# Kernel optimization log

Measured on AMD Instinct MI355X. Metric: run time of the kernel, lower is better.

## Reference

```python
import jax, jax.numpy as jnp
import numpy as np

B, NQ, NN, EMB, H, D = 64, 256, 512, 128, 8, 16
SQRT_EMB = float(np.sqrt(EMB))
LOGIT_CLIP = 10.0


def setup_inputs() -> dict:
    key = jax.random.key(0)
    ks = jax.random.split(key, 9)
    encoded_last_node = jax.random.normal(ks[0], (B, NQ, EMB), jnp.float32)
    attr = jax.random.uniform(ks[1], (B, NQ, 1), jnp.float32)  # e.g. remaining load in [0,1]
    encoded_nodes = jax.random.normal(ks[2], (B, NN, EMB), jnp.float32)
    ninf_mask = jnp.where(jax.random.uniform(ks[3], (B, NQ, NN)) < 0.15,
                          -jnp.inf, 0.0).astype(jnp.float32)
    def lin(k, fan_in, fan_out):
        lim = 1.0 / np.sqrt(fan_in)
        return jax.random.uniform(k, (fan_in, fan_out), jnp.float32, -lim, lim)
    Wq_last = lin(ks[4], EMB + 1, H * D)
    Wk = lin(ks[5], EMB, H * D)
    Wv = lin(ks[6], EMB, H * D)
    Wcomb = lin(ks[7], H * D, EMB)
    bcomb = jax.random.uniform(ks[8], (EMB,), jnp.float32, -1.0 / np.sqrt(H * D), 1.0 / np.sqrt(H * D))
    return dict(encoded_last_node=encoded_last_node, attr=attr,
                encoded_nodes=encoded_nodes, ninf_mask=ninf_mask,
                Wq_last=Wq_last, Wk=Wk, Wv=Wv, Wcomb=Wcomb, bcomb=bcomb)


def _heads(x):  # [B, T, H*D] -> [B, H, T, D]
    return x.reshape(x.shape[0], x.shape[1], H, D).transpose(0, 2, 1, 3)


def reference(encoded_last_node, attr, encoded_nodes, ninf_mask,
              Wq_last, Wk, Wv, Wcomb, bcomb):
    # fix fully-masked rows: un-mask index 0 (matches torch mask_inf patch)
    all_inf = jnp.isinf(ninf_mask).all(axis=2)  # [B, NQ]
    ninf_mask = ninf_mask.at[:, :, 0].set(jnp.where(all_inf, 0.0, ninf_mask[:, :, 0]))

    # set_kv
    k = _heads(encoded_nodes @ Wk)  # [B,H,NN,D]
    v = _heads(encoded_nodes @ Wv)  # [B,H,NN,D]

    # q from last node + attr
    q = _heads(jnp.concatenate([encoded_last_node, attr], axis=2) @ Wq_last)  # [B,H,NQ,D]

    # masked multi-head attention
    score = jnp.einsum('bhnd,bhmd->bhnm', q, k) / jnp.sqrt(jnp.float32(D))
    score = score + ninf_mask[:, None, :, :]          # rank3 mask broadcast over heads
    weights = jax.nn.softmax(score, axis=-1)          # [B,H,NQ,NN]
    out = jnp.einsum('bhnm,bhmd->bhnd', weights, v)
    out_concat = out.transpose(0, 2, 1, 3).reshape(B, NQ, H * D)
    mh_atten_out = out_concat @ Wcomb + bcomb         # [B,NQ,EMB]

    # single-head compatibility score + tanh clip + mask + softmax
    score2 = jnp.einsum('bne,bme->bnm', mh_atten_out, encoded_nodes) / SQRT_EMB
    logits = LOGIT_CLIP * jnp.tanh(score2) + ninf_mask
    probs = jax.nn.softmax(logits, axis=2)            # [B,NQ,NN]
    return probs
```

## Files before the change

### kernel.cpp

```cpp
#include <hip/hip_runtime.h>
#include <math.h>

#define NB    64
#define NQn   256
#define NNn   512
#define HDn   128
#define LOG2E 1.44269504088896340736f
#define INV_SQRT_EMB 0.08838834764831845f

__device__ __forceinline__ float4 ldg4(const float* p) {
    return *reinterpret_cast<const float4*>(p);
}

__global__ __launch_bounds__(256, 4)
void mask_transpose(const float* __restrict__ mask, unsigned char* __restrict__ maskT8)
{
    __shared__ float Ms[64 * 65];
    const int tid = threadIdx.x;
    const int b   = blockIdx.x;
    const int q0  = blockIdx.y * 64;
    const int n0  = blockIdx.z * 64;
    const int qg  = tid >> 6;
    const int ln  = tid & 63;

    #pragma unroll
    for (int j = 0; j < 16; ++j) {
        int q = qg * 16 + j;
        Ms[q * 65 + ln] = mask[((size_t)(b * NQn + q0 + q)) * NNn + n0 + ln];
    }
    __syncthreads();

    const int n  = tid >> 2;
    const int qc = (tid & 3) * 16;
    unsigned int u[4] = {0u, 0u, 0u, 0u};
    #pragma unroll
    for (int j = 0; j < 16; ++j) {
        float v = Ms[(qc + j) * 65 + n];
        unsigned int bit = (v != 0.0f) ? 1u : 0u;
        u[j >> 2] |= bit << (8 * (j & 3));
    }
    *reinterpret_cast<uint4*>(maskT8 + ((size_t)(b * NNn + n0 + n)) * NQn + q0 + qc) =
        make_uint4(u[0], u[1], u[2], u[3]);
}

__global__ __launch_bounds__(256, 2)
void proj_kernel(const float* __restrict__ X,
                 const float* __restrict__ W0, const float* __restrict__ W1,
                 const float* __restrict__ wrow, const float* __restrict__ attr,
                 const float* __restrict__ bias,
                 float* __restrict__ Y0, float* __restrict__ Y1)
{
    __shared__ float Xs[64 * 128];
    __shared__ float Wt[64 * 128];
    const int tid = threadIdx.x;
    const int rg = tid >> 4;
    const int cg = tid & 15;
    const int rowblk = blockIdx.x * 64;
    const int colbase = blockIdx.y * 64;

    #pragma unroll
    for (int i = 0; i < 8; ++i) {
        int idx = tid + 256 * i;
        int r = idx >> 5;
        int c4 = idx & 31;
        float4 v = ldg4(X + (rowblk + r) * 128 + c4 * 4);
        *reinterpret_cast<float4*>(&Xs[r * 128 + ((c4 ^ (r & 7)) << 2)]) = v;
    }

    for (int pass = 0; pass < 2; ++pass) {
        if (pass && (W1 == nullptr)) break;
        const float* W = pass ? W1 : W0;
        float* Y = pass ? Y1 : Y0;
        __syncthreads();
        #pragma unroll
        for (int i = 0; i < 32; ++i) {
            int idx = tid + 256 * i;
            int k = idx >> 6;
            int c = idx & 63;
            float w = W[k * 128 + colbase + c];
            Wt[c * 128 + ((((k >> 2) ^ (c & 7)) << 2) | (k & 3))] = w;
        }
        __syncthreads();

        float acc[4][4];
        #pragma unroll
        for (int r = 0; r < 4; ++r)
            #pragma unroll
            for (int c = 0; c < 4; ++c) acc[r][c] = 0.f;

        const int rsw = rg & 7;
        const int csw = cg & 7;
        #pragma unroll 8
        for (int k4 = 0; k4 < 32; ++k4) {
            float4 a[4], bv[4];
            #pragma unroll
            for (int r = 0; r < 4; ++r)
                a[r] = *reinterpret_cast<const float4*>(&Xs[(rg + 16 * r) * 128 + ((k4 ^ rsw) << 2)]);
            #pragma unroll
            for (int c = 0; c < 4; ++c)
                bv[c] = *reinterpret_cast<const float4*>(&Wt[(cg + 16 * c) * 128 + ((k4 ^ csw) << 2)]);
            #pragma unroll
            for (int r = 0; r < 4; ++r)
                #pragma unroll
                for (int c = 0; c < 4; ++c)
                    acc[r][c] += a[r].x * bv[c].x + a[r].y * bv[c].y
                               + a[r].z * bv[c].z + a[r].w * bv[c].w;
        }

        if (attr != nullptr) {
            #pragma unroll
            for (int r = 0; r < 4; ++r) {
                float av = attr[rowblk + rg + 16 * r];
                #pragma unroll
                for (int c = 0; c < 4; ++c)
                    acc[r][c] += av * wrow[colbase + cg + 16 * c];
            }
        }
        #pragma unroll
        for (int r = 0; r < 4; ++r) {
            int row = rowblk + rg + 16 * r;
            #pragma unroll
            for (int c = 0; c < 4; ++c) {
                int col = colbase + cg + 16 * c;
                float o = acc[r][c];
                if (bias != nullptr) o += bias[col];
                Y[row * 128 + col] = o;
            }
        }
    }
}

__global__ __launch_bounds__(256, 2)
void attn_kernel(const float* __restrict__ Q, const float* __restrict__ K,
                 const float* __restrict__ V, const unsigned int* __restrict__ maskTu,
                 float* __restrict__ P0, float* __restrict__ P1,
                 float* __restrict__ P2, float* __restrict__ P3,
                 float* __restrict__ L0, float* __restrict__ L1,
                 float* __restrict__ L2, float* __restrict__ L3)
{
    __shared__ float Ks[32 * 128];
    __shared__ float Vs[32 * 128];
    const int tid  = threadIdx.x;
    const int lane = tid & 63;
    const int h    = blockIdx.z * 4 + (tid >> 6);
    const int b    = blockIdx.x;
    const int ns   = blockIdx.y;
    const int nbase = ns * 128;

    float qv[4][16];
    {
        const float sc = 0.25f * LOG2E;
        #pragma unroll
        for (int qq = 0; qq < 4; ++qq) {
            const float* qp = Q + ((size_t)(b * NQn + 4 * lane + qq)) * 128 + h * 16;
            #pragma unroll
            for (int j = 0; j < 4; ++j) {
                float4 tv = ldg4(qp + 4 * j);
                qv[qq][4 * j + 0] = tv.x * sc;
                qv[qq][4 * j + 1] = tv.y * sc;
                qv[qq][4 * j + 2] = tv.z * sc;
                qv[qq][4 * j + 3] = tv.w * sc;
            }
        }
    }

    float out[4][16];
    #pragma unroll
    for (int qq = 0; qq < 4; ++qq)
        #pragma unroll
        for (int d = 0; d < 16; ++d) out[qq][d] = 0.f;
    float ls[4] = {0.f, 0.f, 0.f, 0.f};

    const unsigned int* mbase = maskTu + (((size_t)(b * NNn + nbase) * NQn) >> 2) + lane;

    const float* kg = K + ((size_t)(b * NNn + nbase)) * 128;
    const float* vg = V + ((size_t)(b * NNn + nbase)) * 128;

    float4 krp[4], vrp[4];
    #pragma unroll
    for (int i = 0; i < 4; ++i) {
        krp[i] = ldg4(kg + (tid + 256 * i) * 4);
        vrp[i] = ldg4(vg + (tid + 256 * i) * 4);
    }

    for (int t = 0; t < 4; ++t) {
        __syncthreads();
        #pragma unroll
        for (int i = 0; i < 4; ++i) {
            *reinterpret_cast<float4*>(&Ks[(tid + 256 * i) * 4]) = krp[i];
            *reinterpret_cast<float4*>(&Vs[(tid + 256 * i) * 4]) = vrp[i];
        }
        __syncthreads();
        if (t < 3) {
            const float* kg2 = kg + (t + 1) * 32 * 128;
            const float* vg2 = vg + (t + 1) * 32 * 128;
            #pragma unroll
            for (int i = 0; i < 4; ++i) {
                krp[i] = ldg4(kg2 + (tid + 256 * i) * 4);
                vrp[i] = ldg4(vg2 + (tid + 256 * i) * 4);
            }
        }

        const float* kbase = &Ks[h * 16];
        const float* vbase = &Vs[h * 16];
        for (int n = 0; n < 32; ++n) {
            const float* kr = kbase + n * 128;
            const float* vr = vbase + n * 128;
            float kf[16], vf[16];
            *reinterpret_cast<float4*>(&kf[0])  = *reinterpret_cast<const float4*>(kr);
            *reinterpret_cast<float4*>(&kf[4])  = *reinterpret_cast<const float4*>(kr + 4);
            *reinterpret_cast<float4*>(&kf[8])  = *reinterpret_cast<const float4*>(kr + 8);
            *reinterpret_cast<float4*>(&kf[12]) = *reinterpret_cast<const float4*>(kr + 12);
            *reinterpret_cast<float4*>(&vf[0])  = *reinterpret_cast<const float4*>(vr);
            *reinterpret_cast<float4*>(&vf[4])  = *reinterpret_cast<const float4*>(vr + 4);
            *reinterpret_cast<float4*>(&vf[8])  = *reinterpret_cast<const float4*>(vr + 8);
            *reinterpret_cast<float4*>(&vf[12]) = *reinterpret_cast<const float4*>(vr + 12);
            unsigned int m4 = mbase[(t * 32 + n) * (NQn / 4)];

            float p[4];
            #pragma unroll
            for (int qq = 0; qq < 4; ++qq) {
                float aP = qv[qq][0]*kf[0] + qv[qq][1]*kf[1] + qv[qq][2]*kf[2] + qv[qq][3]*kf[3];
                float aQ = qv[qq][4]*kf[4] + qv[qq][5]*kf[5] + qv[qq][6]*kf[6] + qv[qq][7]*kf[7];
                float aR = qv[qq][8]*kf[8] + qv[qq][9]*kf[9] + qv[qq][10]*kf[10] + qv[qq][11]*kf[11];
                float aS = qv[qq][12]*kf[12] + qv[qq][13]*kf[13] + qv[qq][14]*kf[14] + qv[qq][15]*kf[15];
                p[qq] = __builtin_amdgcn_exp2f((aP + aQ) + (aR + aS));
            }
            p[0] = (m4 & 0x000000ffu) ? 0.f : p[0];
            p[1] = (m4 & 0x0000ff00u) ? 0.f : p[1];
            p[2] = (m4 & 0x00ff0000u) ? 0.f : p[2];
            p[3] = (m4 & 0xff000000u) ? 0.f : p[3];
            ls[0] += p[0]; ls[1] += p[1]; ls[2] += p[2]; ls[3] += p[3];
            #pragma unroll
            for (int d = 0; d < 16; ++d) {
                out[0][d] += p[0] * vf[d];
                out[1][d] += p[1] * vf[d];
                out[2][d] += p[2] * vf[d];
                out[3][d] += p[3] * vf[d];
            }
        }
    }

    float* P = (ns == 0) ? P0 : (ns == 1) ? P1 : (ns == 2) ? P2 : P3;
    float* L = (ns == 0) ? L0 : (ns == 1) ? L1 : (ns == 2) ? L2 : L3;
    #pragma unroll
    for (int qq = 0; qq < 4; ++qq) {
        float* op = P + ((size_t)(b * NQn + 4 * lane + qq)) * 128 + h * 16;
        *reinterpret_cast<float4*>(op)      = make_float4(out[qq][0],  out[qq][1],  out[qq][2],  out[qq][3]);
        *reinterpret_cast<float4*>(op + 4)  = make_float4(out[qq][4],  out[qq][5],  out[qq][6],  out[qq][7]);
        *reinterpret_cast<float4*>(op + 8)  = make_float4(out[qq][8],  out[qq][9],  out[qq][10], out[qq][11]);
        *reinterpret_cast<float4*>(op + 12) = make_float4(out[qq][12], out[qq][13], out[qq][14], out[qq][15]);
        L[(b * NQn + 4 * lane + qq) * 8 + h] = ls[qq];
    }
}

__global__ __launch_bounds__(256, 2)
void proj_comb_kernel(const float* __restrict__ P0, const float* __restrict__ P1,
                      const float* __restrict__ P2, const float* __restrict__ P3,
                      const float* __restrict__ L0, const float* __restrict__ L1,
                      const float* __restrict__ L2, const float* __restrict__ L3,
                      const float* __restrict__ V,
                      const float* __restrict__ W0, const float* __restrict__ bias,
                      float* __restrict__ Y0)
{
    __shared__ float Xs[64 * 128];
    __shared__ float Wt[64 * 128];
    const int tid = threadIdx.x;
    const int rg = tid >> 4;
    const int cg = tid & 15;
    const int rowblk = blockIdx.x * 64;
    const int colbase = blockIdx.y * 64;

    #pragma unroll
    for (int i = 0; i < 8; ++i) {
        int idx = tid + 256 * i;
        int r = idx >> 5;
        int c4 = idx & 31;
        int row = rowblk + r;
        int hh = c4 >> 2;
        float l = (L0[row * 8 + hh] + L1[row * 8 + hh])
                + (L2[row * 8 + hh] + L3[row * 8 + hh]);
        float4 v;
        if (l == 0.0f) {
            v = ldg4(V + ((size_t)(row >> 8)) * NNn * 128 + c4 * 4);
        } else {
            float4 a = ldg4(P0 + (size_t)row * 128 + c4 * 4);
            float4 c = ldg4(P1 + (size_t)row * 128 + c4 * 4);
            float4 d = ldg4(P2 + (size_t)row * 128 + c4 * 4);
            float4 e = ldg4(P3 + (size_t)row * 128 + c4 * 4);
            float inv = __builtin_amdgcn_rcpf(l);
            v = make_float4((a.x + c.x + d.x + e.x) * inv,
                            (a.y + c.y + d.y + e.y) * inv,
                            (a.z + c.z + d.z + e.z) * inv,
                            (a.w + c.w + d.w + e.w) * inv);
        }
        *reinterpret_cast<float4*>(&Xs[r * 128 + ((c4 ^ (r & 7)) << 2)]) = v;
    }

    __syncthreads();
    #pragma unroll
    for (int i = 0; i < 32; ++i) {
        int idx = tid + 256 * i;
        int k = idx >> 6;
        int c = idx & 63;
        float w = W0[k * 128 + colbase + c];
        Wt[c * 128 + ((((k >> 2) ^ (c & 7)) << 2) | (k & 3))] = w;
    }
    __syncthreads();

    float acc[4][4];
    #pragma unroll
    for (int r = 0; r < 4; ++r)
        #pragma unroll
        for (int c = 0; c < 4; ++c) acc[r][c] = 0.f;

    const int rsw = rg & 7;
    const int csw = cg & 7;
    #pragma unroll 8
    for (int k4 = 0; k4 < 32; ++k4) {
        float4 a[4], bv[4];
        #pragma unroll
        for (int r = 0; r < 4; ++r)
            a[r] = *reinterpret_cast<const float4*>(&Xs[(rg + 16 * r) * 128 + ((k4 ^ rsw) << 2)]);
        #pragma unroll
        for (int c = 0; c < 4; ++c)
            bv[c] = *reinterpret_cast<const float4*>(&Wt[(cg + 16 * c) * 128 + ((k4 ^ csw) << 2)]);
        #pragma unroll
        for (int r = 0; r < 4; ++r)
            #pragma unroll
            for (int c = 0; c < 4; ++c)
                acc[r][c] += a[r].x * bv[c].x + a[r].y * bv[c].y
                           + a[r].z * bv[c].z + a[r].w * bv[c].w;
    }

    #pragma unroll
    for (int r = 0; r < 4; ++r) {
        int row = rowblk + rg + 16 * r;
        #pragma unroll
        for (int c = 0; c < 4; ++c) {
            int col = colbase + cg + 16 * c;
            Y0[row * 128 + col] = acc[r][c] + bias[col];
        }
    }
}

__global__ __launch_bounds__(512, 4)
void final_kernel(const float* __restrict__ MH, const float* __restrict__ EN,
                  const float* __restrict__ mask, float* __restrict__ OUT)
{
    __shared__ float ENs[128 * 128];
    const int tid = threadIdx.x;
    const int qg = tid >> 4;
    const int mg = tid & 15;
    const int b  = blockIdx.x >> 3;
    const int q0 = (blockIdx.x & 7) * 32;

    const float* mhrow = MH + (b * NQn + q0 + qg) * 128;
    float pr[32];
    float psum = 0.f;
    const int msw = mg & 7;

    #pragma unroll
    for (int t = 0; t < 4; ++t) {
        const int m0 = t * 128;
        __syncthreads();
        #pragma unroll
        for (int i = 0; i < 8; ++i) {
            int idx = tid + 512 * i;
            int r = idx >> 5;
            int c4 = idx & 31;
            float4 v = ldg4(EN + (b * NNn + m0 + r) * 128 + c4 * 4);
            *reinterpret_cast<float4*>(&ENs[r * 128 + ((c4 ^ (r & 7)) << 2)]) = v;
        }
        __syncthreads();

        float acc[8];
        #pragma unroll
        for (int c = 0; c < 8; ++c) acc[c] = 0.f;

        #pragma unroll 4
        for (int k4 = 0; k4 < 32; ++k4) {
            float4 a0 = ldg4(mhrow + k4 * 4);
            float4 bv[8];
            #pragma unroll
            for (int c = 0; c < 8; ++c)
                bv[c] = *reinterpret_cast<const float4*>(&ENs[(mg + 16 * c) * 128 + ((k4 ^ msw) << 2)]);
            #pragma unroll
            for (int c = 0; c < 8; ++c)
                acc[c] += a0.x*bv[c].x + a0.y*bv[c].y + a0.z*bv[c].z + a0.w*bv[c].w;
        }

        const float* mrow = mask + (b * NQn + q0 + qg) * NNn + m0;
        #pragma unroll
        for (int c = 0; c < 8; ++c) {
            int m = mg + 16 * c;
            float s2 = acc[c] * INV_SQRT_EMB;
            float e  = __builtin_amdgcn_exp2f(s2 * (2.0f * LOG2E));
            float rc = __builtin_amdgcn_rcpf(e + 1.0f);
            float mv = mrow[m];
            float pv = __builtin_amdgcn_exp2f((mv - 20.0f * rc) * LOG2E);
            pr[t * 8 + c] = pv;
            psum += pv;
        }
    }

    {
        float s = psum;
        s += __shfl_xor(s, 1);
        s += __shfl_xor(s, 2);
        s += __shfl_xor(s, 4);
        s += __shfl_xor(s, 8);
        psum = s;
    }

    float* orow = OUT + (b * NQn + q0 + qg) * NNn;
    if (psum == 0.0f) {
        #pragma unroll
        for (int t = 0; t < 4; ++t)
            #pragma unroll
            for (int c = 0; c < 8; ++c) {
                int m = t * 128 + mg + 16 * c;
                orow[m] = (m == 0) ? 1.0f : 0.0f;
            }
    } else {
        float inv = __builtin_amdgcn_rcpf(psum);
        #pragma unroll
        for (int t = 0; t < 4; ++t)
            #pragma unroll
            for (int c = 0; c < 8; ++c)
                orow[t * 128 + mg + 16 * c] = pr[t * 8 + c] * inv;
    }
}

extern "C" void kernel_launch(void* const* d_in, const int* in_sizes, int n_in,
                              void* d_out, int out_size, void* d_ws, size_t ws_size,
                              hipStream_t stream) {
    const float* enc_last  = (const float*)d_in[0];
    const float* attr      = (const float*)d_in[1];
    const float* enc_nodes = (const float*)d_in[2];
    const float* mask      = (const float*)d_in[3];
    const float* Wq        = (const float*)d_in[4];
    const float* Wk        = (const float*)d_in[5];
    const float* Wv        = (const float*)d_in[6];
    const float* Wcomb     = (const float*)d_in[7];
    const float* bcomb     = (const float*)d_in[8];
    float* out = (float*)d_out;

    float* Kbuf = (float*)d_ws;
    float* Vbuf = Kbuf + (size_t)NB * NNn * 128;
    float* Qbuf = Vbuf + (size_t)NB * NNn * 128;
    float* P0   = Qbuf + (size_t)NB * NQn * 128;
    float* P1   = P0   + (size_t)NB * NQn * 128;
    float* P2   = P1   + (size_t)NB * NQn * 128;
    float* P3   = P2   + (size_t)NB * NQn * 128;
    float* L0   = P3   + (size_t)NB * NQn * 128;
    float* L1   = L0   + (size_t)NB * NQn * 8;
    float* L2   = L1   + (size_t)NB * NQn * 8;
    float* L3   = L2   + (size_t)NB * NQn * 8;
    unsigned char* maskT8 = (unsigned char*)(L3 + (size_t)NB * NQn * 8);
    float* MH   = Qbuf;

    mask_transpose<<<dim3(NB, NQn / 64, NNn / 64), 256, 0, stream>>>(mask, maskT8);
    proj_kernel<<<dim3(NB * NNn / 64, 2), 256, 0, stream>>>(
        enc_nodes, Wk, Wv, nullptr, nullptr, nullptr, Kbuf, Vbuf);
    proj_kernel<<<dim3(NB * NQn / 64, 2), 256, 0, stream>>>(
        enc_last, Wq, nullptr, Wq + 128 * 128, attr, nullptr, Qbuf, nullptr);
    attn_kernel<<<dim3(NB, 4, 2), 256, 0, stream>>>(
        Qbuf, Kbuf, Vbuf, (const unsigned int*)maskT8,
        P0, P1, P2, P3, L0, L1, L2, L3);
    proj_comb_kernel<<<dim3(NB * NQn / 64, 2), 256, 0, stream>>>(
        P0, P1, P2, P3, L0, L1, L2, L3, Vbuf, Wcomb, bcomb, MH);
    final_kernel<<<dim3(NB * NQn / 32), 512, 0, stream>>>(
        MH, enc_nodes, mask, out);
}
```

Before: 248.7 us.

## Split attention over 8 node chunks with all heads per block, enlarge final blocks

The attention kernel now runs all 8 heads in one 512-thread block. Each block loads a shared K/V tile once for every head instead of twice across two head-halves, and the work is split over up to 8 node chunks when the workspace allows it. The register prefetch double-buffering is removed in favour of a direct load-sync-compute loop. The combine kernel sums a variable number of partials, and the final kernel uses 1024-thread blocks covering 64 queries so each staged encoded-node tile is reused by more rows. The risks are lower occupancy from the larger blocks with heavy register use, more partial traffic to reduce, and exposed load latency now that prefetch is gone.

```diff
diff --git a/kernel.cpp b/kernel.cpp
--- a/kernel.cpp
+++ b/kernel.cpp
@@ -130,22 +130,19 @@
     }
 }
 
-__global__ __launch_bounds__(256, 2)
+__global__ __launch_bounds__(512, 2)
 void attn_kernel(const float* __restrict__ Q, const float* __restrict__ K,
                  const float* __restrict__ V, const unsigned int* __restrict__ maskTu,
-                 float* __restrict__ P0, float* __restrict__ P1,
-                 float* __restrict__ P2, float* __restrict__ P3,
-                 float* __restrict__ L0, float* __restrict__ L1,
-                 float* __restrict__ L2, float* __restrict__ L3)
+                 float* __restrict__ Pbase, float* __restrict__ Lbase, int ntiles)
 {
     __shared__ float Ks[32 * 128];
     __shared__ float Vs[32 * 128];
     const int tid  = threadIdx.x;
     const int lane = tid & 63;
-    const int h    = blockIdx.z * 4 + (tid >> 6);
+    const int h    = tid >> 6;
     const int b    = blockIdx.x;
     const int ns   = blockIdx.y;
-    const int nbase = ns * 128;
+    const int nbase = ns * (ntiles * 32);
 
     float qv[4][16];
     {
@@ -173,33 +170,21 @@
 
     const unsigned int* mbase = maskTu + (((size_t)(b * NNn + nbase) * NQn) >> 2) + lane;
 
-    const float* kg = K + ((size_t)(b * NNn + nbase)) * 128;
-    const float* vg = V + ((size_t)(b * NNn + nbase)) * 128;
-
-    float4 krp[4], vrp[4];
-    #pragma unroll
-    for (int i = 0; i < 4; ++i) {
-        krp[i] = ldg4(kg + (tid + 256 * i) * 4);
-        vrp[i] = ldg4(vg + (tid + 256 * i) * 4);
-    }
-
-    for (int t = 0; t < 4; ++t) {
-        __syncthreads();
-        #pragma unroll
-        for (int i = 0; i < 4; ++i) {
-            *reinterpret_cast<float4*>(&Ks[(tid + 256 * i) * 4]) = krp[i];
-            *reinterpret_cast<float4*>(&Vs[(tid + 256 * i) * 4]) = vrp[i];
-        }
-        __syncthreads();
-        if (t < 3) {
-            const float* kg2 = kg + (t + 1) * 32 * 128;
-            const float* vg2 = vg + (t + 1) * 32 * 128;
-            #pragma unroll
-            for (int i = 0; i < 4; ++i) {
-                krp[i] = ldg4(kg2 + (tid + 256 * i) * 4);
-                vrp[i] = ldg4(vg2 + (tid + 256 * i) * 4);
-            }
-        }
+    for (int t = 0; t < ntiles; ++t) {
+        __syncthreads();
+        {
+            const float* kg = K + ((size_t)(b * NNn + nbase + t * 32)) * 128;
+            const float* vg = V + ((size_t)(b * NNn + nbase + t * 32)) * 128;
+            float4 k0 = ldg4(kg + tid * 4);
+            float4 k1 = ldg4(kg + (tid + 512) * 4);
+            float4 v0 = ldg4(vg + tid * 4);
+            float4 v1 = ldg4(vg + (tid + 512) * 4);
+            *reinterpret_cast<float4*>(&Ks[tid * 4]) = k0;
+            *reinterpret_cast<float4*>(&Ks[(tid + 512) * 4]) = k1;
+            *reinterpret_cast<float4*>(&Vs[tid * 4]) = v0;
+            *reinterpret_cast<float4*>(&Vs[(tid + 512) * 4]) = v1;
+        }
+        __syncthreads();
 
         const float* kbase = &Ks[h * 16];
         const float* vbase = &Vs[h * 16];
@@ -241,8 +226,8 @@
         }
     }
 
-    float* P = (ns == 0) ? P0 : (ns == 1) ? P1 : (ns == 2) ? P2 : P3;
-    float* L = (ns == 0) ? L0 : (ns == 1) ? L1 : (ns == 2) ? L2 : L3;
+    float* P = Pbase + (size_t)ns * NB * NQn * 128;
+    float* L = Lbase + (size_t)ns * NB * NQn * 8;
     #pragma unroll
     for (int qq = 0; qq < 4; ++qq) {
         float* op = P + ((size_t)(b * NQn + 4 * lane + qq)) * 128 + h * 16;
@@ -255,11 +240,8 @@
 }
 
 __global__ __launch_bounds__(256, 2)
-void proj_comb_kernel(const float* __restrict__ P0, const float* __restrict__ P1,
-                      const float* __restrict__ P2, const float* __restrict__ P3,
-                      const float* __restrict__ L0, const float* __restrict__ L1,
-                      const float* __restrict__ L2, const float* __restrict__ L3,
-                      const float* __restrict__ V,
+void proj_comb_kernel(const float* __restrict__ Pbase, const float* __restrict__ Lbase,
+                      int nsplit, const float* __restrict__ V,
                       const float* __restrict__ W0, const float* __restrict__ bias,
                       float* __restrict__ Y0)
 {
@@ -270,6 +252,8 @@
     const int cg = tid & 15;
     const int rowblk = blockIdx.x * 64;
     const int colbase = blockIdx.y * 64;
+    const size_t PS = (size_t)NB * NQn * 128;
+    const size_t LS = (size_t)NB * NQn * 8;
 
     #pragma unroll
     for (int i = 0; i < 8; ++i) {
@@ -278,21 +262,20 @@
         int c4 = idx & 31;
         int row = rowblk + r;
         int hh = c4 >> 2;
-        float l = (L0[row * 8 + hh] + L1[row * 8 + hh])
-                + (L2[row * 8 + hh] + L3[row * 8 + hh]);
+        float l = 0.f;
+        for (int s = 0; s < nsplit; ++s)
+            l += Lbase[s * LS + row * 8 + hh];
         float4 v;
         if (l == 0.0f) {
             v = ldg4(V + ((size_t)(row >> 8)) * NNn * 128 + c4 * 4);
         } else {
-            float4 a = ldg4(P0 + (size_t)row * 128 + c4 * 4);
-            float4 c = ldg4(P1 + (size_t)row * 128 + c4 * 4);
-            float4 d = ldg4(P2 + (size_t)row * 128 + c4 * 4);
-            float4 e = ldg4(P3 + (size_t)row * 128 + c4 * 4);
+            float sx = 0.f, sy = 0.f, sz = 0.f, sw = 0.f;
+            for (int s = 0; s < nsplit; ++s) {
+                float4 a = ldg4(Pbase + s * PS + (size_t)row * 128 + c4 * 4);
+                sx += a.x; sy += a.y; sz += a.z; sw += a.w;
+            }
             float inv = __builtin_amdgcn_rcpf(l);
-            v = make_float4((a.x + c.x + d.x + e.x) * inv,
-                            (a.y + c.y + d.y + e.y) * inv,
-                            (a.z + c.z + d.z + e.z) * inv,
-                            (a.w + c.w + d.w + e.w) * inv);
+            v = make_float4(sx * inv, sy * inv, sz * inv, sw * inv);
         }
         *reinterpret_cast<float4*>(&Xs[r * 128 + ((c4 ^ (r & 7)) << 2)]) = v;
     }
@@ -344,7 +327,7 @@
     }
 }
 
-__global__ __launch_bounds__(512, 4)
+__global__ __launch_bounds__(1024, 4)
 void final_kernel(const float* __restrict__ MH, const float* __restrict__ EN,
                   const float* __restrict__ mask, float* __restrict__ OUT)
 {
@@ -352,8 +335,8 @@
     const int tid = threadIdx.x;
     const int qg = tid >> 4;
     const int mg = tid & 15;
-    const int b  = blockIdx.x >> 3;
-    const int q0 = (blockIdx.x & 7) * 32;
+    const int b  = blockIdx.x >> 2;
+    const int q0 = (blockIdx.x & 3) * 64;
 
     const float* mhrow = MH + (b * NQn + q0 + qg) * 128;
     float pr[32];
@@ -365,8 +348,8 @@
         const int m0 = t * 128;
         __syncthreads();
         #pragma unroll
-        for (int i = 0; i < 8; ++i) {
-            int idx = tid + 512 * i;
+        for (int i = 0; i < 4; ++i) {
+            int idx = tid + 1024 * i;
             int r = idx >> 5;
             int c4 = idx & 31;
             float4 v = ldg4(EN + (b * NNn + m0 + r) * 128 + c4 * 4);
@@ -446,30 +429,30 @@
     const float* bcomb     = (const float*)d_in[8];
     float* out = (float*)d_out;
 
-    float* Kbuf = (float*)d_ws;
-    float* Vbuf = Kbuf + (size_t)NB * NNn * 128;
-    float* Qbuf = Vbuf + (size_t)NB * NNn * 128;
-    float* P0   = Qbuf + (size_t)NB * NQn * 128;
-    float* P1   = P0   + (size_t)NB * NQn * 128;
-    float* P2   = P1   + (size_t)NB * NQn * 128;
-    float* P3   = P2   + (size_t)NB * NQn * 128;
-    float* L0   = P3   + (size_t)NB * NQn * 128;
-    float* L1   = L0   + (size_t)NB * NQn * 8;
-    float* L2   = L1   + (size_t)NB * NQn * 8;
-    float* L3   = L2   + (size_t)NB * NQn * 8;
-    unsigned char* maskT8 = (unsigned char*)(L3 + (size_t)NB * NQn * 8);
-    float* MH   = Qbuf;
+    const size_t PS = (size_t)NB * NQn * 128;
+    const size_t LS = (size_t)NB * NQn * 8;
+    const size_t KVQ = (size_t)NB * NNn * 128 * 2 + (size_t)NB * NQn * 128;
+    const size_t need8 = (KVQ + 8 * (PS + LS)) * 4 + (size_t)NB * NNn * NQn;
+    const int nsplit = (ws_size >= need8) ? 8 : 4;
+    const int ntiles = (nsplit == 8) ? 2 : 4;
+
+    float* Kbuf  = (float*)d_ws;
+    float* Vbuf  = Kbuf + (size_t)NB * NNn * 128;
+    float* Qbuf  = Vbuf + (size_t)NB * NNn * 128;
+    float* Pbase = Qbuf + (size_t)NB * NQn * 128;
+    float* Lbase = Pbase + (size_t)nsplit * PS;
+    unsigned char* maskT8 = (unsigned char*)(Lbase + (size_t)nsplit * LS);
+    float* MH    = Qbuf;
 
     mask_transpose<<<dim3(NB, NQn / 64, NNn / 64), 256, 0, stream>>>(mask, maskT8);
     proj_kernel<<<dim3(NB * NNn / 64, 2), 256, 0, stream>>>(
         enc_nodes, Wk, Wv, nullptr, nullptr, nullptr, Kbuf, Vbuf);
     proj_kernel<<<dim3(NB * NQn / 64, 2), 256, 0, stream>>>(
         enc_last, Wq, nullptr, Wq + 128 * 128, attr, nullptr, Qbuf, nullptr);
-    attn_kernel<<<dim3(NB, 4, 2), 256, 0, stream>>>(
-        Qbuf, Kbuf, Vbuf, (const unsigned int*)maskT8,
-        P0, P1, P2, P3, L0, L1, L2, L3);
+    attn_kernel<<<dim3(NB, nsplit), 512, 0, stream>>>(
+        Qbuf, Kbuf, Vbuf, (const unsigned int*)maskT8, Pbase, Lbase, ntiles);
     proj_comb_kernel<<<dim3(NB * NQn / 64, 2), 256, 0, stream>>>(
-        P0, P1, P2, P3, L0, L1, L2, L3, Vbuf, Wcomb, bcomb, MH);
-    final_kernel<<<dim3(NB * NQn / 32), 512, 0, stream>>>(
+        Pbase, Lbase, nsplit, Vbuf, Wcomb, bcomb, MH);
+    final_kernel<<<dim3(NB * NQn / 64), 1024, 0, stream>>>(
         MH, enc_nodes, mask, out);
 }
```

New measurement: 282.8 us. 13.7% more time.
